# Performance work log

Hardware: AMD Instinct MI355X
Metric: run time of the kernel (lower is better)

## Reference

```python
import jax, jax.numpy as jnp
import numpy as np


def setup_inputs() -> dict:
    key = jax.random.key(0)
    k1, k2 = jax.random.split(key)
    B, H, W, D, C = 4, 128, 128, 128, 2
    image = jax.random.normal(k1, (B, H, W, D, C), dtype=jnp.float32)
    # near-identity affine so sampling is meaningful (localization-net output stand-in)
    theta = 0.1 * jax.random.normal(k2, (B, 3, 4), dtype=jnp.float32) + jnp.eye(3, 4, dtype=jnp.float32)[None]
    return {"image": image, "theta": theta}


def reference(image, theta):
    # Faithful port of SpatialTransformer._transform / _interpolate (incl. its
    # original index-flattening and z-weight (z1 - z0) conventions).
    B, H, W, D, C = image.shape
    oH, oW, oD = H, W, D  # downsample_factor = 1
    N = oH * oW * oD

    # _meshgrid: tf.meshgrid default 'xy' indexing -> shapes (oH, oW, oD)
    xl = jnp.linspace(-1.0, 1.0, oW)
    yl = jnp.linspace(-1.0, 1.0, oH)
    zl = jnp.linspace(-1.0, 1.0, oD)
    Xg, Yg, Zg = jnp.meshgrid(xl, yl, zl)
    grid = jnp.stack([Xg.ravel(), Yg.ravel(), Zg.ravel(), jnp.ones(N, jnp.float32)], 0)  # [4, N]

    tg = jnp.einsum('bij,jn->bin', theta.astype(jnp.float32), grid)  # [B, 3, N]
    x = tg[:, 0, :].reshape(-1)
    y = tg[:, 1, :].reshape(-1)
    z = tg[:, 2, :].reshape(-1)

    # map from [-1, 1] to pixel coords (original uses full extent, not extent-1)
    x = 0.5 * (x + 1.0) * W
    y = 0.5 * (y + 1.0) * H
    z = 0.5 * (z + 1.0) * D

    x0 = jnp.floor(x).astype(jnp.int32); x1 = x0 + 1
    y0 = jnp.floor(y).astype(jnp.int32); y1 = y0 + 1
    z0 = jnp.floor(z).astype(jnp.int32); z1 = z0 + 1
    x0 = jnp.clip(x0, 0, W - 1); x1 = jnp.clip(x1, 0, W - 1)
    y0 = jnp.clip(y0, 0, H - 1); y1 = jnp.clip(y1, 0, H - 1)
    z0 = jnp.clip(z0, 0, D - 1); z1 = jnp.clip(z1, 0, D - 1)

    base = jnp.repeat(jnp.arange(B, dtype=jnp.int32) * (H * W * D), N)  # [B*N]
    # original flat-index convention: base + y*W + z*W*H + x
    b00 = base + y0 * W + z0 * (W * H)
    b10 = base + y1 * W + z0 * (W * H)
    b01 = base + y0 * W + z1 * (W * H)
    b11 = base + y1 * W + z1 * (W * H)

    flat = image.reshape(-1, C).astype(jnp.float32)  # [B*H*W*D, C]
    pa = flat[b00 + x0]; pb = flat[b10 + x0]
    pc = flat[b00 + x1]; pd = flat[b10 + x1]
    pe = flat[b01 + x0]; pf = flat[b11 + x0]
    pg = flat[b01 + x1]; ph = flat[b11 + x1]

    x0f = x0.astype(jnp.float32); x1f = x1.astype(jnp.float32)
    y0f = y0.astype(jnp.float32); y1f = y1.astype(jnp.float32)
    z0f = z0.astype(jnp.float32); z1f = z1.astype(jnp.float32)

    wa = ((x1f - x) * (y1f - y) * (z1f - z))[:, None]
    wb = ((x1f - x) * (y - y0f) * (z1f - z))[:, None]
    wc = ((x - x0f) * (y1f - y) * (z1f - z))[:, None]
    wd = ((x - x0f) * (y - y0f) * (z1f - z))[:, None]
    we = ((x1f - x) * (y1f - y) * (z1f - z0f))[:, None]
    wf = ((x1f - x) * (y - y0f) * (z1f - z0f))[:, None]
    wg = ((x - x0f) * (y1f - y) * (z1f - z0f))[:, None]
    wh = ((x - x0f) * (y - y0f) * (z1f - z0f))[:, None]

    out = (wa * pa + wb * pb + wc * pc + wd * pd
           + we * pe + wf * pf + wg * pg + wh * ph)  # [B*N, C]
    return out.reshape(B, oH, oW, oD, C)
```

## Files before the change

### kernel.cpp

```cpp
#include <hip/hip_runtime.h>
#include <math.h>

#define BN 4
#define HN 128
#define WN 128
#define DN 128

__global__ __launch_bounds__(256) void st_trilerp_kernel(
    const float* __restrict__ image,
    const float* __restrict__ theta,
    float* __restrict__ out)
{
    const int bi = blockIdx.z;
    const int b  = bi >> 7;
    const int i  = bi & (HN - 1);
    const int j0 = blockIdx.y << 4;
    const int k0 = blockIdx.x << 4;

    const int tid = threadIdx.x;
    const int jj = tid & 15;
    const int kk = tid >> 4;
    const int j = j0 + jj;
    const int k = k0 + kk;

    const double step = 2.0 / 127.0;
    const double X = (j == WN - 1) ? 1.0 : (double)j * step - 1.0;
    const double Y = (i == HN - 1) ? 1.0 : (double)i * step - 1.0;
    const double Z = (k == DN - 1) ? 1.0 : (double)k * step - 1.0;

    const float* th = theta + b * 12;
    const double xt = (((double)th[0] * X + (double)th[1] * Y) + (double)th[2]  * Z) + (double)th[3];
    const double yt = (((double)th[4] * X + (double)th[5] * Y) + (double)th[6]  * Z) + (double)th[7];
    const double zt = (((double)th[8] * X + (double)th[9] * Y) + (double)th[10] * Z) + (double)th[11];

    const double x = (0.5 * (xt + 1.0)) * (double)WN;
    const double y = (0.5 * (yt + 1.0)) * (double)HN;
    const double z = (0.5 * (zt + 1.0)) * (double)DN;

    const int x0u = (int)floor(x);
    const int y0u = (int)floor(y);
    const int z0u = (int)floor(z);
    const int x0 = min(max(x0u,     0), WN - 1);
    const int x1 = min(max(x0u + 1, 0), WN - 1);
    const int y0 = min(max(y0u,     0), HN - 1);
    const int y1 = min(max(y0u + 1, 0), HN - 1);
    const int z0 = min(max(z0u,     0), DN - 1);
    const int z1 = min(max(z0u + 1, 0), DN - 1);

    const int base = b * (HN * WN * DN);
    const int b00 = base + y0 * WN + z0 * (WN * HN);
    const int b10 = base + y1 * WN + z0 * (WN * HN);
    const int b01 = base + y0 * WN + z1 * (WN * HN);
    const int b11 = base + y1 * WN + z1 * (WN * HN);

    const float2* __restrict__ img2 = (const float2*)image;

    const int xb = min(x0, WN - 2);
    const bool lo0 = (x0 == xb);
    const bool lo1 = (x1 == xb);

    const float4 q00 = *(const float4*)(img2 + b00 + xb);
    const float4 q10 = *(const float4*)(img2 + b10 + xb);
    const float4 q01 = *(const float4*)(img2 + b01 + xb);
    const float4 q11 = *(const float4*)(img2 + b11 + xb);

    const float2 pa = lo0 ? make_float2(q00.x, q00.y) : make_float2(q00.z, q00.w);
    const float2 pc = lo1 ? make_float2(q00.x, q00.y) : make_float2(q00.z, q00.w);
    const float2 pb = lo0 ? make_float2(q10.x, q10.y) : make_float2(q10.z, q10.w);
    const float2 pd = lo1 ? make_float2(q10.x, q10.y) : make_float2(q10.z, q10.w);
    const float2 pe = lo0 ? make_float2(q01.x, q01.y) : make_float2(q01.z, q01.w);
    const float2 pg = lo1 ? make_float2(q01.x, q01.y) : make_float2(q01.z, q01.w);
    const float2 pf = lo0 ? make_float2(q11.x, q11.y) : make_float2(q11.z, q11.w);
    const float2 ph = lo1 ? make_float2(q11.x, q11.y) : make_float2(q11.z, q11.w);

    const float wx0 = (float)((double)x1 - x), wx1 = (float)(x - (double)x0);
    const float wy0 = (float)((double)y1 - y), wy1 = (float)(y - (double)y0);
    const float wz0 = (float)((double)z1 - z);
    const float wzA = (float)(z1 - z0);

    const float wa = wx0 * wy0 * wz0;
    const float wb = wx0 * wy1 * wz0;
    const float wc = wx1 * wy0 * wz0;
    const float wd = wx1 * wy1 * wz0;
    const float we = wx0 * wy0 * wzA;
    const float wf = wx0 * wy1 * wzA;
    const float wg = wx1 * wy0 * wzA;
    const float wh = wx1 * wy1 * wzA;

    float2 o;
    o.x = wa * pa.x + wb * pb.x + wc * pc.x + wd * pd.x
        + we * pe.x + wf * pf.x + wg * pg.x + wh * ph.x;
    o.y = wa * pa.y + wb * pb.y + wc * pc.y + wd * pd.y
        + we * pe.y + wf * pf.y + wg * pg.y + wh * ph.y;

    __shared__ float2 tile[16][17];
    tile[kk][jj] = o;
    __syncthreads();

    const int kw = tid & 15;
    const int jw = tid >> 4;
    const int oidx = (bi * WN + (j0 + jw)) * DN + (k0 + kw);
    ((float2*)out)[oidx] = tile[kw][jw];
}

extern "C" void kernel_launch(void* const* d_in, const int* in_sizes, int n_in,
                              void* d_out, int out_size, void* d_ws, size_t ws_size,
                              hipStream_t stream) {
    const float* image = (const float*)d_in[0];
    const float* theta = (const float*)d_in[1];
    float* out = (float*)d_out;

    dim3 grid(DN / 16, WN / 16, BN * HN);
    st_trilerp_kernel<<<grid, 256, 0, stream>>>(image, theta, out);
}
```

Measured before the change: 145.1 us.

## Process two depth rows per thread, pre-convert theta to double, factor trilinear weights

Each thread now computes two output voxels along the depth axis, so the block tile grows to 32x16 and the grid halves. Per-thread X/Y setup is shared between the two voxels. A tiny pre-kernel converts theta to double in the workspace so the main kernel skips repeated float-to-double conversions. The interpolation is refactored to fold the x-weights into low/high lane weights, which removes the per-corner selects and trims FMAs. The extra launch adds a small fixed overhead, and the larger tile raises register and shared-memory use.

```diff
diff --git a/kernel.cpp b/kernel.cpp
--- a/kernel.cpp
+++ b/kernel.cpp
@@ -6,101 +6,112 @@
 #define WN 128
 #define DN 128
 
+__global__ void theta_cvt_kernel(const float* __restrict__ theta,
+                                 double* __restrict__ thd) {
+    const int t = threadIdx.x;
+    if (t < BN * 12) thd[t] = (double)theta[t];
+}
+
 __global__ __launch_bounds__(256) void st_trilerp_kernel(
     const float* __restrict__ image,
-    const float* __restrict__ theta,
+    const double* __restrict__ thd,
     float* __restrict__ out)
 {
     const int bi = blockIdx.z;
     const int b  = bi >> 7;
     const int i  = bi & (HN - 1);
     const int j0 = blockIdx.y << 4;
-    const int k0 = blockIdx.x << 4;
+    const int k0 = blockIdx.x << 5;
 
     const int tid = threadIdx.x;
-    const int jj = tid & 15;
-    const int kk = tid >> 4;
+    const int jj  = tid & 15;
+    const int kk0 = tid >> 4;
     const int j = j0 + jj;
-    const int k = k0 + kk;
 
     const double step = 2.0 / 127.0;
     const double X = (j == WN - 1) ? 1.0 : (double)j * step - 1.0;
     const double Y = (i == HN - 1) ? 1.0 : (double)i * step - 1.0;
-    const double Z = (k == DN - 1) ? 1.0 : (double)k * step - 1.0;
 
-    const float* th = theta + b * 12;
-    const double xt = (((double)th[0] * X + (double)th[1] * Y) + (double)th[2]  * Z) + (double)th[3];
-    const double yt = (((double)th[4] * X + (double)th[5] * Y) + (double)th[6]  * Z) + (double)th[7];
-    const double zt = (((double)th[8] * X + (double)th[9] * Y) + (double)th[10] * Z) + (double)th[11];
+    const double* th = thd + b * 12;
 
-    const double x = (0.5 * (xt + 1.0)) * (double)WN;
-    const double y = (0.5 * (yt + 1.0)) * (double)HN;
-    const double z = (0.5 * (zt + 1.0)) * (double)DN;
+    __shared__ float2 tile[32][17];
+    const float2* __restrict__ img2 = (const float2*)image;
+    const int base = b * (HN * WN * DN);
 
-    const int x0u = (int)floor(x);
-    const int y0u = (int)floor(y);
-    const int z0u = (int)floor(z);
-    const int x0 = min(max(x0u,     0), WN - 1);
-    const int x1 = min(max(x0u + 1, 0), WN - 1);
-    const int y0 = min(max(y0u,     0), HN - 1);
-    const int y1 = min(max(y0u + 1, 0), HN - 1);
-    const int z0 = min(max(z0u,     0), DN - 1);
-    const int z1 = min(max(z0u + 1, 0), DN - 1);
+#pragma unroll
+    for (int v = 0; v < 2; ++v) {
+        const int kk = kk0 + v * 16;
+        const int k = k0 + kk;
+        const double Z = (k == DN - 1) ? 1.0 : (double)k * step - 1.0;
 
-    const int base = b * (HN * WN * DN);
-    const int b00 = base + y0 * WN + z0 * (WN * HN);
-    const int b10 = base + y1 * WN + z0 * (WN * HN);
-    const int b01 = base + y0 * WN + z1 * (WN * HN);
-    const int b11 = base + y1 * WN + z1 * (WN * HN);
+        const double xt = ((th[0] * X + th[1] * Y) + th[2]  * Z) + th[3];
+        const double yt = ((th[4] * X + th[5] * Y) + th[6]  * Z) + th[7];
+        const double zt = ((th[8] * X + th[9] * Y) + th[10] * Z) + th[11];
 
-    const float2* __restrict__ img2 = (const float2*)image;
+        const double x = (0.5 * (xt + 1.0)) * (double)WN;
+        const double y = (0.5 * (yt + 1.0)) * (double)HN;
+        const double z = (0.5 * (zt + 1.0)) * (double)DN;
 
-    const int xb = min(x0, WN - 2);
-    const bool lo0 = (x0 == xb);
-    const bool lo1 = (x1 == xb);
+        const int x0u = (int)floor(x);
+        const int y0u = (int)floor(y);
+        const int z0u = (int)floor(z);
+        const int x0 = min(max(x0u,     0), WN - 1);
+        const int x1 = min(max(x0u + 1, 0), WN - 1);
+        const int y0 = min(max(y0u,     0), HN - 1);
+        const int y1 = min(max(y0u + 1, 0), HN - 1);
+        const int z0 = min(max(z0u,     0), DN - 1);
+        const int z1 = min(max(z0u + 1, 0), DN - 1);
 
-    const float4 q00 = *(const float4*)(img2 + b00 + xb);
-    const float4 q10 = *(const float4*)(img2 + b10 + xb);
-    const float4 q01 = *(const float4*)(img2 + b01 + xb);
-    const float4 q11 = *(const float4*)(img2 + b11 + xb);
+        const int b00 = base + y0 * WN + z0 * (WN * HN);
+        const int b10 = base + y1 * WN + z0 * (WN * HN);
+        const int b01 = base + y0 * WN + z1 * (WN * HN);
+        const int b11 = base + y1 * WN + z1 * (WN * HN);
 
-    const float2 pa = lo0 ? make_float2(q00.x, q00.y) : make_float2(q00.z, q00.w);
-    const float2 pc = lo1 ? make_float2(q00.x, q00.y) : make_float2(q00.z, q00.w);
-    const float2 pb = lo0 ? make_float2(q10.x, q10.y) : make_float2(q10.z, q10.w);
-    const float2 pd = lo1 ? make_float2(q10.x, q10.y) : make_float2(q10.z, q10.w);
-    const float2 pe = lo0 ? make_float2(q01.x, q01.y) : make_float2(q01.z, q01.w);
-    const float2 pg = lo1 ? make_float2(q01.x, q01.y) : make_float2(q01.z, q01.w);
-    const float2 pf = lo0 ? make_float2(q11.x, q11.y) : make_float2(q11.z, q11.w);
-    const float2 ph = lo1 ? make_float2(q11.x, q11.y) : make_float2(q11.z, q11.w);
+        const int xb = min(x0, WN - 2);
+        const bool lo0 = (x0 == xb);
+        const bool lo1 = (x1 == xb);
 
-    const float wx0 = (float)((double)x1 - x), wx1 = (float)(x - (double)x0);
-    const float wy0 = (float)((double)y1 - y), wy1 = (float)(y - (double)y0);
-    const float wz0 = (float)((double)z1 - z);
-    const float wzA = (float)(z1 - z0);
+        const float4 q00 = *(const float4*)(img2 + b00 + xb);
+        const float4 q10 = *(const float4*)(img2 + b10 + xb);
+        const float4 q01 = *(const float4*)(img2 + b01 + xb);
+        const float4 q11 = *(const float4*)(img2 + b11 + xb);
 
-    const float wa = wx0 * wy0 * wz0;
-    const float wb = wx0 * wy1 * wz0;
-    const float wc = wx1 * wy0 * wz0;
-    const float wd = wx1 * wy1 * wz0;
-    const float we = wx0 * wy0 * wzA;
-    const float wf = wx0 * wy1 * wzA;
-    const float wg = wx1 * wy0 * wzA;
-    const float wh = wx1 * wy1 * wzA;
+        const float wx0 = (float)((double)x1 - x), wx1 = (float)(x - (double)x0);
+        const float wy0 = (float)((double)y1 - y), wy1 = (float)(y - (double)y0);
+        const float wz0 = (float)((double)z1 - z);
+        const float wzA = (float)(z1 - z0);
 
-    float2 o;
-    o.x = wa * pa.x + wb * pb.x + wc * pc.x + wd * pd.x
-        + we * pe.x + wf * pf.x + wg * pg.x + wh * ph.x;
-    o.y = wa * pa.y + wb * pb.y + wc * pc.y + wd * pd.y
-        + we * pe.y + wf * pf.y + wg * pg.y + wh * ph.y;
+        const float wxl = (lo0 ? wx0 : 0.0f) + (lo1 ? wx1 : 0.0f);
+        const float wxh = (lo0 ? 0.0f : wx0) + (lo1 ? 0.0f : wx1);
 
-    __shared__ float2 tile[16][17];
-    tile[kk][jj] = o;
+        const float s00 = wy0 * wz0;
+        const float s10 = wy1 * wz0;
+        const float s01 = wy0 * wzA;
+        const float s11 = wy1 * wzA;
+
+        float2 o;
+        o.x = s00 * (wxl * q00.x + wxh * q00.z)
+            + s10 * (wxl * q10.x + wxh * q10.z)
+            + s01 * (wxl * q01.x + wxh * q01.z)
+            + s11 * (wxl * q11.x + wxh * q11.z);
+        o.y = s00 * (wxl * q00.y + wxh * q00.w)
+            + s10 * (wxl * q10.y + wxh * q10.w)
+            + s01 * (wxl * q01.y + wxh * q01.w)
+            + s11 * (wxl * q11.y + wxh * q11.w);
+
+        tile[kk][jj] = o;
+    }
+
     __syncthreads();
 
-    const int kw = tid & 15;
-    const int jw = tid >> 4;
-    const int oidx = (bi * WN + (j0 + jw)) * DN + (k0 + kw);
-    ((float2*)out)[oidx] = tile[kw][jw];
+#pragma unroll
+    for (int v = 0; v < 2; ++v) {
+        const int wid = tid + v * 256;
+        const int kw = wid & 31;
+        const int jw = wid >> 5;
+        const int oidx = (bi * WN + (j0 + jw)) * DN + (k0 + kw);
+        ((float2*)out)[oidx] = tile[kw][jw];
+    }
 }
 
 extern "C" void kernel_launch(void* const* d_in, const int* in_sizes, int n_in,
@@ -109,7 +120,10 @@
     const float* image = (const float*)d_in[0];
     const float* theta = (const float*)d_in[1];
     float* out = (float*)d_out;
+    double* thd = (double*)d_ws;
 
-    dim3 grid(DN / 16, WN / 16, BN * HN);
-    st_trilerp_kernel<<<grid, 256, 0, stream>>>(image, theta, out);
+    theta_cvt_kernel<<<1, 64, 0, stream>>>(theta, thd);
+
+    dim3 grid(DN / 32, WN / 16, BN * HN);
+    st_trilerp_kernel<<<grid, 256, 0, stream>>>(image, thd, out);
 }
```

Result: no change. 146.7 us (+1.1%).
